# Kernel optimization log

Measured on AMD Instinct MI355X. Metric: run time of the kernel, lower is better.

Reference implementation:

```python
import jax, jax.numpy as jnp
import numpy as np

V, E, H, L = 10000, 256, 512, 2
B, T, S = 64, 64, 128
NEG = -1e6


def setup_inputs() -> dict:
    key = jax.random.key(0)
    ks = jax.random.split(key, 20)
    sc = 0.02
    inp = {
        "x": jax.random.randint(ks[0], (B, T), 0, V),
        "enc_outputs": jax.random.normal(ks[1], (B, S, H), jnp.float32),
        "h0": jax.random.normal(ks[2], (L, B, H), jnp.float32),
        "valid_lens": jax.random.randint(ks[3], (B,), 1, S + 1).astype(jnp.int32),
        # params
        "emb": jax.random.normal(ks[4], (V, E), jnp.float32) * sc,
        "Wq": jax.random.normal(ks[5], (H, H), jnp.float32) * sc,
        "Wk": jax.random.normal(ks[6], (H, H), jnp.float32) * sc,
        "wv": jax.random.normal(ks[7], (H,), jnp.float32) * sc,
        "W_ih0": jax.random.normal(ks[8], (3 * H, H + E), jnp.float32) * sc,
        "W_hh0": jax.random.normal(ks[9], (3 * H, H), jnp.float32) * sc,
        "b_ih0": jnp.zeros((3 * H,), jnp.float32),
        "b_hh0": jnp.zeros((3 * H,), jnp.float32),
        "W_ih1": jax.random.normal(ks[10], (3 * H, H), jnp.float32) * sc,
        "W_hh1": jax.random.normal(ks[11], (3 * H, H), jnp.float32) * sc,
        "b_ih1": jnp.zeros((3 * H,), jnp.float32),
        "b_hh1": jnp.zeros((3 * H,), jnp.float32),
        "Wd": jax.random.normal(ks[12], (V, H), jnp.float32) * sc,
        "bd": jnp.zeros((V,), jnp.float32),
    }
    return inp


def _gru_cell(x, h, W_ih, W_hh, b_ih, b_hh):
    # PyTorch GRU cell math
    gi = x @ W_ih.T + b_ih  # (B, 3H)
    gh = h @ W_hh.T + b_hh
    ir, iz, in_ = jnp.split(gi, 3, axis=-1)
    hr, hz, hn = jnp.split(gh, 3, axis=-1)
    r = jax.nn.sigmoid(ir + hr)
    z = jax.nn.sigmoid(iz + hz)
    n = jnp.tanh(in_ + r * hn)
    return (1.0 - z) * n + z * h


def reference(x, enc_outputs, h0, valid_lens, emb, Wq, Wk, wv,
              W_ih0, W_hh0, b_ih0, b_hh0, W_ih1, W_hh1, b_ih1, b_hh1, Wd, bd):
    X = emb[x]                     # (B, T, E)
    Xt = jnp.transpose(X, (1, 0, 2))  # (T, B, E) time-major
    k_proj = jnp.einsum('bsh,oh->bso', enc_outputs, Wk)  # precompute W_k(keys)
    mask = jnp.arange(S)[None, :] < valid_lens[:, None]  # (B, S)

    def step(h, x_t):
        q = h[-1]                                      # (B, H) last-layer hidden
        q_proj = q @ Wq.T                              # (B, H)
        feats = jnp.tanh(q_proj[:, None, :] + k_proj)  # (B, S, H)
        scores = jnp.einsum('bsh,h->bs', feats, wv)
        scores = jnp.where(mask, scores, NEG)
        attn = jax.nn.softmax(scores, axis=-1)
        context = jnp.einsum('bs,bsh->bh', attn, enc_outputs)
        inp = jnp.concatenate([context, x_t], axis=-1)  # (B, H+E)
        h0n = _gru_cell(inp, h[0], W_ih0, W_hh0, b_ih0, b_hh0)
        h1n = _gru_cell(h0n, h[1], W_ih1, W_hh1, b_ih1, b_hh1)
        hn = jnp.stack([h0n, h1n])
        return hn, h1n

    _, ys = jax.lax.scan(step, h0, Xt)       # ys: (T, B, H)
    logits = jnp.einsum('tbh,vh->tbv', ys, Wd) + bd
    return jnp.transpose(logits, (1, 0, 2))  # (B, T, V)
```

## Files before the change

kernel.cpp:

```cpp
#include <hip/hip_runtime.h>
#include <hip/hip_bf16.h>

#define Bd 64
#define Td 64
#define Sd 128
#define Hd 512
#define Ed 256
#define Vd 10000
#define NBLK 256

#define W0IH 0
#define W0HH 4608
#define W1IH 7680
#define W1HH 10752
#define WTOT 13824

typedef __attribute__((ext_vector_type(8))) short bf16x8;
typedef __attribute__((ext_vector_type(4))) float f32x4;

__device__ __forceinline__ float fast_tanh(float x) {
  float e = __expf(-2.0f * fabsf(x));
  float r = (1.0f - e) / (1.0f + e);
  return copysignf(r, x);
}
__device__ __forceinline__ float fast_sigmoid(float x) {
  return 1.0f / (1.0f + __expf(-x));
}
__device__ __forceinline__ float bf2f(unsigned short u) {
  return __uint_as_float(((unsigned int)u) << 16);
}
__device__ __forceinline__ void st_llc(float* p, float v) {
  __hip_atomic_store(p, v, __ATOMIC_RELAXED, __HIP_MEMORY_SCOPE_AGENT);
}
__device__ __forceinline__ int q4(int k, int b) {
  return (k >> 2) * 256 + b * 4 + (k & 3);
}

__device__ __forceinline__ void gbar(int* arrive, int* go, int ep, int blk, int tid) {
  __syncthreads();
  if (tid == 0)
    __hip_atomic_store(&arrive[blk], ep, __ATOMIC_RELAXED, __HIP_MEMORY_SCOPE_AGENT);
  if (blk == 0) {
    if (tid < 64) {
      for (;;) {
        int a0 = __hip_atomic_load(&arrive[tid], __ATOMIC_RELAXED,
                                   __HIP_MEMORY_SCOPE_AGENT);
        int a1 = __hip_atomic_load(&arrive[tid + 64], __ATOMIC_RELAXED,
                                   __HIP_MEMORY_SCOPE_AGENT);
        int a2 = __hip_atomic_load(&arrive[tid + 128], __ATOMIC_RELAXED,
                                   __HIP_MEMORY_SCOPE_AGENT);
        int a3 = __hip_atomic_load(&arrive[tid + 192], __ATOMIC_RELAXED,
                                   __HIP_MEMORY_SCOPE_AGENT);
        if (a0 >= ep && a1 >= ep && a2 >= ep && a3 >= ep) break;
        __builtin_amdgcn_s_sleep(2);
      }
    }
    __syncthreads();
    if (tid == 0)
      __hip_atomic_store(go, ep, __ATOMIC_RELAXED, __HIP_MEMORY_SCOPE_AGENT);
  }
  if (tid == 0) {
    while (__hip_atomic_load(go, __ATOMIC_RELAXED, __HIP_MEMORY_SCOPE_AGENT) < ep) {
      __builtin_amdgcn_s_sleep(1);
    }
    __builtin_amdgcn_fence(__ATOMIC_ACQUIRE, "agent");
  }
  __syncthreads();
}

__global__ void k_gemm_kp(const float* __restrict__ A, const float* __restrict__ W,
                          unsigned short* __restrict__ C, int M, int N, int K) {
  __shared__ __align__(16) float As[16][64];
  __shared__ __align__(16) float Ws[16][64];
  int m0 = blockIdx.x * 64, n0 = blockIdx.y * 64;
  int tid = threadIdx.x;
  int tx = tid & 15, ty = tid >> 4;
  float acc[4][4] = {};
  for (int k0 = 0; k0 < K; k0 += 16) {
#pragma unroll
    for (int i = 0; i < 4; i++) {
      int e = tid + i * 256;
      int r = e >> 4, c = e & 15;
      As[c][r] = A[(long)(m0 + r) * K + k0 + c];
      Ws[c][r] = W[(long)(n0 + r) * K + k0 + c];
    }
    __syncthreads();
#pragma unroll
    for (int k = 0; k < 16; k++) {
      float a_[4], w_[4];
#pragma unroll
      for (int i = 0; i < 4; i++) a_[i] = As[k][ty * 4 + i];
#pragma unroll
      for (int j = 0; j < 4; j++) w_[j] = Ws[k][tx * 4 + j];
#pragma unroll
      for (int i = 0; i < 4; i++)
#pragma unroll
        for (int j = 0; j < 4; j++) acc[i][j] += a_[i] * w_[j];
    }
    __syncthreads();
  }
#pragma unroll
  for (int i = 0; i < 4; i++)
#pragma unroll
    for (int j = 0; j < 4; j++) {
      __hip_bfloat16 h = __float2bfloat16(acc[i][j]);
      C[(long)(m0 + ty * 4 + i) * N + n0 + tx * 4 + j] = *(unsigned short*)&h;
    }
}

__global__ __launch_bounds__(256) void k_logits(
    const unsigned short* __restrict__ ysbf, const unsigned short* __restrict__ Wdbf,
    const float* __restrict__ bd, float* __restrict__ out, int N) {
  int m0 = blockIdx.x * 64, n0 = blockIdx.y * 64;
  int w = threadIdx.x >> 6, lane = threadIdx.x & 63;
  int row = lane & 15, kg = lane >> 4;
  int mw = m0 + w * 16;
  f32x4 acc[4] = {};
  const unsigned short* Arow = ysbf + (size_t)(mw + row) * 512 + kg * 8;
  for (int k0 = 0; k0 < 512; k0 += 32) {
    bf16x8 af = *(const bf16x8*)(Arow + k0);
#pragma unroll
    for (int nn = 0; nn < 4; nn++) {
      int ncol = n0 + nn * 16 + row;
      bf16x8 bfv = {};
      if (ncol < N) bfv = *(const bf16x8*)(Wdbf + (size_t)ncol * 512 + k0 + kg * 8);
      acc[nn] = __builtin_amdgcn_mfma_f32_16x16x32_bf16(af, bfv, acc[nn], 0, 0, 0);
    }
  }
#pragma unroll
  for (int nn = 0; nn < 4; nn++) {
    int ncol = n0 + nn * 16 + row;
    if (ncol < N) {
      float bv = bd[ncol];
#pragma unroll
      for (int r = 0; r < 4; r++) {
        int mm = mw + kg * 4 + r;
        int t_ = mm >> 6, b_ = mm & 63;
        out[((size_t)(b_ * Td + t_)) * N + ncol] = acc[nn][r] + bv;
      }
    }
  }
}

__global__ void k_tobf(const float* __restrict__ src, unsigned short* __restrict__ dst,
                       long n) {
  long i = (long)blockIdx.x * 1024 + threadIdx.x;
  if (i < n) {
    __hip_bfloat16 h = __float2bfloat16(src[i]);
    dst[i] = *(unsigned short*)&h;
  }
}

__global__ void k_embT(const int* __restrict__ x, const float* __restrict__ emb,
                       float* __restrict__ embTf) {
  __shared__ int rows[64];
  int t = blockIdx.x;
  if (threadIdx.x < 64) rows[threadIdx.x] = x[threadIdx.x * Td + t];
  __syncthreads();
  int e = threadIdx.x;
  for (int b = 0; b < 64; b++) {
    embTf[(size_t)t * 16384 + q4(e, b)] = emb[(long)rows[b] * Ed + e];
  }
}

template <bool C0>
__device__ __forceinline__ void cell_phase(
    int blk, int tid, int t, const float* __restrict__ aT,
    const float* __restrict__ embTf, const float* __restrict__ hT,
    const float* wIH, const float* wHH, const float* __restrict__ bih,
    const float* __restrict__ bhh, const float* __restrict__ dscale,
    float* __restrict__ houtT, unsigned short* __restrict__ ysbf, float* scratch) {
  int lane = tid & 63;
  int w = tid >> 6;
  const int RIH = C0 ? 768 : 512;
  float* ps = scratch;
  float* psE = scratch + 1536;
  if (w < 12) {
    int p = w >> 1, h = w & 1;
    bool ih = p < 3;
    int g = ih ? p : p - 3;
    const float* A = (ih ? aT : hT) + h * 64 * 256;
    const float* w0;
    const float* w1;
    if (ih) {
      w0 = wIH + (size_t)(2 * g) * RIH + h * 256;
      w1 = w0 + RIH;
    } else {
      w0 = wHH + (size_t)(2 * g) * 512 + h * 256;
      w1 = w0 + 512;
    }
    float a0 = 0.f, a1 = 0.f;
#pragma unroll 16
    for (int k = 0; k < 256; k += 4) {
      float4 x0 = *(const float4*)&w0[k];
      float4 x1 = *(const float4*)&w1[k];
      float4 av = *(const float4*)&A[(k >> 2) * 256 + lane * 4];
      a0 += av.x * x0.x + av.y * x0.y + av.z * x0.z + av.w * x0.w;
      a1 += av.x * x1.x + av.y * x1.y + av.z * x1.z + av.w * x1.w;
    }
    if (C0 && ih) {
      float inv = 1.0f / dscale[lane];
      a0 *= inv;
      a1 *= inv;
    }
    int R0 = (ih ? 0 : 6) + 2 * g;
    ps[(R0 * 2 + h) * 64 + lane] = a0;
    ps[((R0 + 1) * 2 + h) * 64 + lane] = a1;
  } else if (C0 && w < 15) {
    int r0 = (w - 12) * 2;
    const float* w0 = wIH + (size_t)r0 * 768 + 512;
    const float* w1 = wIH + (size_t)(r0 + 1) * 768 + 512;
    const float* ef = embTf + (size_t)t * 16384;
    float a0 = 0.f, a1 = 0.f;
#pragma unroll 16
    for (int e = 0; e < 256; e += 4) {
      float4 x0 = *(const float4*)&w0[e];
      float4 x1 = *(const float4*)&w1[e];
      float4 ev = *(const float4*)&ef[(e >> 2) * 256 + lane * 4];
      a0 += ev.x * x0.x + ev.y * x0.y + ev.z * x0.z + ev.w * x0.w;
      a1 += ev.x * x1.x + ev.y * x1.y + ev.z * x1.z + ev.w * x1.w;
    }
    psE[r0 * 64 + lane] = a0;
    psE[(r0 + 1) * 64 + lane] = a1;
  }
  __syncthreads();
  if (tid < 128) {
    int jl = tid >> 6, b = tid & 63;
#define RD(R) (ps[((R)*2 + 0) * 64 + b] + ps[((R)*2 + 1) * 64 + b])
    float ir = RD(0 + jl);
    float iz = RD(2 + jl);
    float in = RD(4 + jl);
    if (C0) {
      ir += psE[(0 + jl) * 64 + b];
      iz += psE[(2 + jl) * 64 + b];
      in += psE[(4 + jl) * 64 + b];
    }
    float hr = RD(6 + jl);
    float hz = RD(8 + jl);
    float hn_ = RD(10 + jl);
#undef RD
    int j = blk * 2 + jl;
    float r = fast_sigmoid(ir + hr + bih[j] + bhh[j]);
    float z = fast_sigmoid(iz + hz + bih[Hd + j] + bhh[Hd + j]);
    float n = fast_tanh(in + bih[2 * Hd + j] + r * (hn_ + bhh[2 * Hd + j]));
    float hp = hT[q4(j, b)];
    float out = (1.f - z) * n + z * hp;
    st_llc(&houtT[q4(j, b)], out);
    if (!C0) {
      __hip_bfloat16 hb = __float2bfloat16(out);
      ysbf[((size_t)t * 64 + b) * 512 + j] = *(unsigned short*)&hb;
    }
  }
}

__global__ __launch_bounds__(1024, 1) void k_decoder(
    const float* __restrict__ h0_in, const int* __restrict__ vlen,
    const float* __restrict__ Wq, const float* __restrict__ wvp,
    const float* __restrict__ Wih0, const float* __restrict__ Whh0,
    const float* __restrict__ bih0, const float* __restrict__ bhh0,
    const float* __restrict__ Wih1, const float* __restrict__ Whh1,
    const float* __restrict__ bih1, const float* __restrict__ bhh1,
    const unsigned short* __restrict__ kpbf, const unsigned short* __restrict__ encbf,
    const float* __restrict__ embTf, int* bar, float* qpN, float* ctxT,
    float* den, float* h0TA, float* h0TB, float* h1TA, float* h1TB,
    unsigned short* ysbf) {
  __shared__ __align__(16) float wLDS[WTOT];
  __shared__ __align__(16) float WqL[1024];
  __shared__ __align__(16) unsigned short kpL[32 * 512];
  __shared__ __align__(16) unsigned short encL[32 * 512];
  __shared__ __align__(16) float scratch[1920];
  int blk = blockIdx.x, tid = threadIdx.x;
  int lane = tid & 63;
  int w = tid >> 6;
  int battn = blk >> 2, q = blk & 3;
  int* arrive = bar;
  int* go = bar + NBLK;
  int ep = 0;

  {
    int j0 = blk * 2;
#pragma unroll
    for (int rr = 0; rr < 6; rr++) {
      int g = rr >> 1, jl = rr & 1;
      int row = g * Hd + j0 + jl;
      const float* s0 = Wih0 + (size_t)row * 768;
      for (int k = tid; k < 768; k += 1024) wLDS[W0IH + rr * 768 + k] = s0[k];
      const float* s1 = Whh0 + (size_t)row * Hd;
      for (int k = tid; k < Hd; k += 1024) wLDS[W0HH + rr * 512 + k] = s1[k];
      const float* s2 = Wih1 + (size_t)row * Hd;
      for (int k = tid; k < Hd; k += 1024) wLDS[W1IH + rr * 512 + k] = s2[k];
      const float* s3 = Whh1 + (size_t)row * Hd;
      for (int k = tid; k < Hd; k += 1024) wLDS[W1HH + rr * 512 + k] = s3[k];
    }
    WqL[tid] = Wq[(size_t)(blk * 2 + (tid >> 9)) * Hd + (tid & 511)];
    const uint4* ksrc = (const uint4*)(kpbf + ((size_t)battn * Sd + q * 32) * Hd);
    const uint4* esrc = (const uint4*)(encbf + ((size_t)battn * Sd + q * 32) * Hd);
    uint4* kdst = (uint4*)kpL;
    uint4* edst = (uint4*)encL;
    for (int i = tid; i < 2048; i += 1024) {
      kdst[i] = ksrc[i];
      edst[i] = esrc[i];
    }
  }
  float wvr[8];
#pragma unroll
  for (int i = 0; i < 8; i++) wvr[i] = wvp[lane * 8 + i];

  if (blk < Bd) {
    int b = blk;
    for (int k = tid; k < Hd; k += 1024) {
      st_llc(&h0TA[q4(k, b)], h0_in[(0 * Bd + b) * Hd + k]);
      st_llc(&h1TA[q4(k, b)], h0_in[(1 * Bd + b) * Hd + k]);
    }
  }
  if (tid < 128) st_llc(&ctxT[blk * 128 + tid], 0.f);
  if (blk < Bd && tid == 128) st_llc(&den[blk], 0.f);
  gbar(arrive, go, ++ep, blk, tid);

  for (int t = 0; t < Td; t++) {
    const float* h0prev = (t & 1) ? h0TB : h0TA;
    float* h0next = (t & 1) ? h0TA : h0TB;
    const float* h1prev = (t & 1) ? h1TB : h1TA;
    float* h1next = (t & 1) ? h1TA : h1TB;

    {
      int rl = w >> 3, ks = w & 7;
      const float* qrow = &WqL[rl * 512 + ks * 64];
      const float* hp4 = h1prev + (ks * 16) * 256 + lane * 4;
      float acc = 0.f;
#pragma unroll
      for (int kk = 0; kk < 64; kk += 4) {
        float4 hv = *(const float4*)&hp4[(kk >> 2) * 256];
        acc += hv.x * qrow[kk] + hv.y * qrow[kk + 1] + hv.z * qrow[kk + 2] +
               hv.w * qrow[kk + 3];
      }
      scratch[w * 64 + lane] = acc;
      __syncthreads();
      if (tid < 128) {
        int rl2 = tid >> 6, b = tid & 63;
        float s = 0.f;
#pragma unroll
        for (int qq = 0; qq < 8; qq++) s += scratch[(rl2 * 8 + qq) * 64 + b];
        st_llc(&qpN[(size_t)b * 512 + blk * 2 + rl2], s);
      }
    }
    gbar(arrive, go, ++ep, blk, tid);

    {
      int b = battn;
      float* sc = scratch;
      float qv[8];
      const float* qb = qpN + (size_t)b * 512 + lane * 8;
#pragma unroll
      for (int i = 0; i < 8; i++) qv[i] = qb[i];
      int vl = vlen[b];
#pragma unroll
      for (int si = 0; si < 2; si++) {
        int sl = w * 2 + si;
        uint4 kw = *(const uint4*)&kpL[sl * 512 + lane * 8];
        float f0 = __uint_as_float(kw.x << 16);
        float f1 = __uint_as_float(kw.x & 0xffff0000u);
        float f2 = __uint_as_float(kw.y << 16);
        float f3 = __uint_as_float(kw.y & 0xffff0000u);
        float f4 = __uint_as_float(kw.z << 16);
        float f5 = __uint_as_float(kw.z & 0xffff0000u);
        float f6 = __uint_as_float(kw.w << 16);
        float f7 = __uint_as_float(kw.w & 0xffff0000u);
        float acc = wvr[0] * fast_tanh(qv[0] + f0) + wvr[1] * fast_tanh(qv[1] + f1) +
                    wvr[2] * fast_tanh(qv[2] + f2) + wvr[3] * fast_tanh(qv[3] + f3) +
                    wvr[4] * fast_tanh(qv[4] + f4) + wvr[5] * fast_tanh(qv[5] + f5) +
                    wvr[6] * fast_tanh(qv[6] + f6) + wvr[7] * fast_tanh(qv[7] + f7);
#pragma unroll
        for (int off = 1; off < 64; off <<= 1) acc += __shfl_xor(acc, off);
        if (lane == 0) {
          int s = q * 32 + sl;
          sc[sl] = (s < vl) ? __expf(acc) : 0.f;
        }
      }
      __syncthreads();
      if (tid < 32) {
        float p2 = sc[tid];
#pragma unroll
        for (int off = 1; off < 32; off <<= 1) p2 += __shfl_xor(p2, off, 32);
        if (tid == 0) atomicAdd(&den[b], p2);
      }
      if (tid < 512) {
        float acc = 0.f;
#pragma unroll 8
        for (int s = 0; s < 32; s++) acc += sc[s] * bf2f(encL[s * 512 + tid]);
        atomicAdd(&ctxT[q4(tid, b)], acc);
      }
    }
    gbar(arrive, go, ++ep, blk, tid);

    cell_phase<true>(blk, tid, t, ctxT, embTf, h0prev, wLDS + W0IH, wLDS + W0HH,
                     bih0, bhh0, den, h0next, nullptr, scratch);
    gbar(arrive, go, ++ep, blk, tid);

    if (tid < 128) st_llc(&ctxT[blk * 128 + tid], 0.f);
    if (blk < Bd && tid == 128) st_llc(&den[blk], 0.f);
    cell_phase<false>(blk, tid, t, h0next, nullptr, h1prev, wLDS + W1IH,
                      wLDS + W1HH, bih1, bhh1, nullptr, h1next, ysbf, scratch);
    gbar(arrive, go, ++ep, blk, tid);
  }
}

extern "C" void kernel_launch(void* const* d_in, const int* in_sizes, int n_in,
                              void* d_out, int out_size, void* d_ws, size_t ws_size,
                              hipStream_t stream) {
  const int* x = (const int*)d_in[0];
  const float* enc = (const float*)d_in[1];
  const float* h0 = (const float*)d_in[2];
  const int* vlen = (const int*)d_in[3];
  const float* emb = (const float*)d_in[4];
  const float* Wq = (const float*)d_in[5];
  const float* Wk = (const float*)d_in[6];
  const float* wv = (const float*)d_in[7];
  const float* W_ih0 = (const float*)d_in[8];
  const float* W_hh0 = (const float*)d_in[9];
  const float* b_ih0 = (const float*)d_in[10];
  const float* b_hh0 = (const float*)d_in[11];
  const float* W_ih1 = (const float*)d_in[12];
  const float* W_hh1 = (const float*)d_in[13];
  const float* b_ih1 = (const float*)d_in[14];
  const float* b_hh1 = (const float*)d_in[15];
  const float* Wd = (const float*)d_in[16];
  const float* bd = (const float*)d_in[17];
  float* out = (float*)d_out;

  char* p = (char*)d_ws;
  int* bar = (int*)p;
  p += 2048;
  unsigned short* kpbf = (unsigned short*)p;
  p += (size_t)Bd * Sd * Hd * 2;
  unsigned short* encbf = (unsigned short*)p;
  p += (size_t)Bd * Sd * Hd * 2;
  unsigned short* Wdbf = (unsigned short*)p;
  p += (size_t)Vd * Hd * 2;
  unsigned short* ysbf = (unsigned short*)p;
  p += (size_t)Td * Bd * Hd * 2;
  float* embTf = (float*)p;
  p += (size_t)Td * Ed * Bd * 4;
  float* qpN = (float*)p;   p += (size_t)Bd * Hd * 4;
  float* ctxT = (float*)p;  p += (size_t)Hd * Bd * 4;
  float* den = (float*)p;   p += 256;
  float* h0TA = (float*)p;  p += (size_t)Hd * Bd * 4;
  float* h0TB = (float*)p;  p += (size_t)Hd * Bd * 4;
  float* h1TA = (float*)p;  p += (size_t)Hd * Bd * 4;
  float* h1TB = (float*)p;

  hipMemsetAsync(bar, 0, 2048, stream);

  k_gemm_kp<<<dim3(128, 8), 256, 0, stream>>>(enc, Wk, kpbf, Bd * Sd, Hd, Hd);
  long nenc = (long)Bd * Sd * Hd;
  k_tobf<<<(nenc + 1023) / 1024, 1024, 0, stream>>>(enc, encbf, nenc);
  long nwd = (long)Vd * Hd;
  k_tobf<<<(nwd + 1023) / 1024, 1024, 0, stream>>>(Wd, Wdbf, nwd);
  k_embT<<<Td, 256, 0, stream>>>(x, emb, embTf);
  k_decoder<<<NBLK, 1024, 0, stream>>>(h0, vlen, Wq, wv, W_ih0, W_hh0, b_ih0,
                                       b_hh0, W_ih1, W_hh1, b_ih1, b_hh1, kpbf,
                                       encbf, embTf, bar, qpN, ctxT, den, h0TA,
                                       h0TB, h1TA, h1TB, ysbf);
  k_logits<<<dim3(64, 157), 256, 0, stream>>>(ysbf, Wdbf, bd, out, Vd);
}
```

Baseline: 4.208 ms.

## Compute query projection redundantly per block to drop a grid barrier

Each block now computes the full 512-wide query projection for its own batch row from a bf16 transposed copy of Wq, which a new prep kernel produces. This removes the distributed qpN write and one grid-wide barrier per timestep. The GRU cell matvec is also restructured: 8 waves each handle 6 rows over a quarter of K, with the attention denominator division applied after the reduction. The cost is redundant Wq reads from global/L2 in every block (four blocks per batch row do the same work), plus bf16 rounding of Wq.

```diff
diff --git a/kernel.cpp b/kernel.cpp
--- a/kernel.cpp
+++ b/kernel.cpp
@@ -151,6 +151,20 @@
   }
 }
 
+__global__ void k_wqT(const float* __restrict__ Wq, unsigned short* __restrict__ WqT) {
+  __shared__ float tile[64][65];
+  int bi = blockIdx.x, bj = blockIdx.y;
+  int tx = threadIdx.x & 63, ty = threadIdx.x >> 6;
+  for (int i = 0; i < 64; i += 4)
+    tile[ty + i][tx] = Wq[(size_t)(bi * 64 + ty + i) * 512 + bj * 64 + tx];
+  __syncthreads();
+  for (int i = 0; i < 64; i += 4) {
+    int r = ty + i;
+    __hip_bfloat16 h = __float2bfloat16(tile[tx][r]);
+    WqT[(size_t)(bj * 64 + r) * 512 + bi * 64 + tx] = *(unsigned short*)&h;
+  }
+}
+
 __global__ void k_embT(const int* __restrict__ x, const float* __restrict__ emb,
                        float* __restrict__ embTf) {
   __shared__ int rows[64];
@@ -168,77 +182,71 @@
     int blk, int tid, int t, const float* __restrict__ aT,
     const float* __restrict__ embTf, const float* __restrict__ hT,
     const float* wIH, const float* wHH, const float* __restrict__ bih,
-    const float* __restrict__ bhh, const float* __restrict__ dscale,
+    const float* __restrict__ bhh, const float* __restrict__ den,
     float* __restrict__ houtT, unsigned short* __restrict__ ysbf, float* scratch) {
   int lane = tid & 63;
   int w = tid >> 6;
   const int RIH = C0 ? 768 : 512;
   float* ps = scratch;
-  float* psE = scratch + 1536;
-  if (w < 12) {
-    int p = w >> 1, h = w & 1;
-    bool ih = p < 3;
-    int g = ih ? p : p - 3;
-    const float* A = (ih ? aT : hT) + h * 64 * 256;
-    const float* w0;
-    const float* w1;
-    if (ih) {
-      w0 = wIH + (size_t)(2 * g) * RIH + h * 256;
-      w1 = w0 + RIH;
-    } else {
-      w0 = wHH + (size_t)(2 * g) * 512 + h * 256;
-      w1 = w0 + 512;
-    }
-    float a0 = 0.f, a1 = 0.f;
-#pragma unroll 16
-    for (int k = 0; k < 256; k += 4) {
-      float4 x0 = *(const float4*)&w0[k];
-      float4 x1 = *(const float4*)&w1[k];
-      float4 av = *(const float4*)&A[(k >> 2) * 256 + lane * 4];
-      a0 += av.x * x0.x + av.y * x0.y + av.z * x0.z + av.w * x0.w;
-      a1 += av.x * x1.x + av.y * x1.y + av.z * x1.z + av.w * x1.w;
-    }
-    if (C0 && ih) {
-      float inv = 1.0f / dscale[lane];
-      a0 *= inv;
-      a1 *= inv;
-    }
-    int R0 = (ih ? 0 : 6) + 2 * g;
-    ps[(R0 * 2 + h) * 64 + lane] = a0;
-    ps[((R0 + 1) * 2 + h) * 64 + lane] = a1;
-  } else if (C0 && w < 15) {
-    int r0 = (w - 12) * 2;
-    const float* w0 = wIH + (size_t)r0 * 768 + 512;
-    const float* w1 = wIH + (size_t)(r0 + 1) * 768 + 512;
-    const float* ef = embTf + (size_t)t * 16384;
-    float a0 = 0.f, a1 = 0.f;
-#pragma unroll 16
-    for (int e = 0; e < 256; e += 4) {
-      float4 x0 = *(const float4*)&w0[e];
-      float4 x1 = *(const float4*)&w1[e];
-      float4 ev = *(const float4*)&ef[(e >> 2) * 256 + lane * 4];
-      a0 += ev.x * x0.x + ev.y * x0.y + ev.z * x0.z + ev.w * x0.w;
-      a1 += ev.x * x1.x + ev.y * x1.y + ev.z * x1.z + ev.w * x1.w;
-    }
-    psE[r0 * 64 + lane] = a0;
-    psE[(r0 + 1) * 64 + lane] = a1;
+  float* psE = scratch + 3072;
+  if (w < 8) {
+    int strm = w >> 2, qk = w & 3;
+    const float* A = (strm == 0 ? aT : hT) + qk * 32 * 256;
+    float a[6] = {0.f, 0.f, 0.f, 0.f, 0.f, 0.f};
+#pragma unroll 8
+    for (int k4 = 0; k4 < 32; k4++) {
+      float4 av = *(const float4*)&A[k4 * 256 + lane * 4];
+#pragma unroll
+      for (int r = 0; r < 6; r++) {
+        const float* wr = (strm == 0 ? wIH + (size_t)r * RIH : wHH + (size_t)r * 512) +
+                          qk * 128 + k4 * 4;
+        float4 w4 = *(const float4*)wr;
+        a[r] += av.x * w4.x + av.y * w4.y + av.z * w4.z + av.w * w4.w;
+      }
+    }
+    int base = strm * 6;
+#pragma unroll
+    for (int r = 0; r < 6; r++) ps[((base + r) * 4 + qk) * 64 + lane] = a[r];
+  } else if (C0 && w < 12) {
+    int qe = w - 8;
+    const float* ef = embTf + (size_t)t * 16384 + qe * 16 * 256;
+    float a[6] = {0.f, 0.f, 0.f, 0.f, 0.f, 0.f};
+#pragma unroll 8
+    for (int k4 = 0; k4 < 16; k4++) {
+      float4 ev = *(const float4*)&ef[k4 * 256 + lane * 4];
+#pragma unroll
+      for (int r = 0; r < 6; r++) {
+        const float* wr = wIH + (size_t)r * 768 + 512 + qe * 64 + k4 * 4;
+        float4 w4 = *(const float4*)wr;
+        a[r] += ev.x * w4.x + ev.y * w4.y + ev.z * w4.z + ev.w * w4.w;
+      }
+    }
+#pragma unroll
+    for (int r = 0; r < 6; r++) psE[(r * 4 + qe) * 64 + lane] = a[r];
   }
   __syncthreads();
   if (tid < 128) {
     int jl = tid >> 6, b = tid & 63;
-#define RD(R) (ps[((R)*2 + 0) * 64 + b] + ps[((R)*2 + 1) * 64 + b])
+    float invd = C0 ? (1.0f / den[b]) : 1.0f;
+#define RD(R)                                                              \
+  (ps[((R)*4 + 0) * 64 + b] + ps[((R)*4 + 1) * 64 + b] +                   \
+   ps[((R)*4 + 2) * 64 + b] + ps[((R)*4 + 3) * 64 + b])
+#define RE(R)                                                              \
+  (psE[((R)*4 + 0) * 64 + b] + psE[((R)*4 + 1) * 64 + b] +                 \
+   psE[((R)*4 + 2) * 64 + b] + psE[((R)*4 + 3) * 64 + b])
     float ir = RD(0 + jl);
     float iz = RD(2 + jl);
     float in = RD(4 + jl);
     if (C0) {
-      ir += psE[(0 + jl) * 64 + b];
-      iz += psE[(2 + jl) * 64 + b];
-      in += psE[(4 + jl) * 64 + b];
+      ir = ir * invd + RE(0 + jl);
+      iz = iz * invd + RE(2 + jl);
+      in = in * invd + RE(4 + jl);
     }
     float hr = RD(6 + jl);
     float hz = RD(8 + jl);
     float hn_ = RD(10 + jl);
 #undef RD
+#undef RE
     int j = blk * 2 + jl;
     float r = fast_sigmoid(ir + hr + bih[j] + bhh[j]);
     float z = fast_sigmoid(iz + hz + bih[Hd + j] + bhh[Hd + j]);
@@ -255,20 +263,19 @@
 
 __global__ __launch_bounds__(1024, 1) void k_decoder(
     const float* __restrict__ h0_in, const int* __restrict__ vlen,
-    const float* __restrict__ Wq, const float* __restrict__ wvp,
+    const unsigned short* __restrict__ WqTbf, const float* __restrict__ wvp,
     const float* __restrict__ Wih0, const float* __restrict__ Whh0,
     const float* __restrict__ bih0, const float* __restrict__ bhh0,
     const float* __restrict__ Wih1, const float* __restrict__ Whh1,
     const float* __restrict__ bih1, const float* __restrict__ bhh1,
     const unsigned short* __restrict__ kpbf, const unsigned short* __restrict__ encbf,
-    const float* __restrict__ embTf, int* bar, float* qpN, float* ctxT,
-    float* den, float* h0TA, float* h0TB, float* h1TA, float* h1TB,
-    unsigned short* ysbf) {
+    const float* __restrict__ embTf, int* bar, float* ctxT, float* den,
+    float* h0TA, float* h0TB, float* h1TA, float* h1TB, unsigned short* ysbf) {
   __shared__ __align__(16) float wLDS[WTOT];
-  __shared__ __align__(16) float WqL[1024];
   __shared__ __align__(16) unsigned short kpL[32 * 512];
   __shared__ __align__(16) unsigned short encL[32 * 512];
-  __shared__ __align__(16) float scratch[1920];
+  __shared__ __align__(16) float scratch[4608];
+  __shared__ __align__(16) float h1s[512];
   int blk = blockIdx.x, tid = threadIdx.x;
   int lane = tid & 63;
   int w = tid >> 6;
@@ -292,7 +299,6 @@
       const float* s3 = Whh1 + (size_t)row * Hd;
       for (int k = tid; k < Hd; k += 1024) wLDS[W1HH + rr * 512 + k] = s3[k];
     }
-    WqL[tid] = Wq[(size_t)(blk * 2 + (tid >> 9)) * Hd + (tid & 511)];
     const uint4* ksrc = (const uint4*)(kpbf + ((size_t)battn * Sd + q * 32) * Hd);
     const uint4* esrc = (const uint4*)(encbf + ((size_t)battn * Sd + q * 32) * Hd);
     uint4* kdst = (uint4*)kpL;
@@ -324,35 +330,42 @@
     float* h1next = (t & 1) ? h1TA : h1TB;
 
     {
-      int rl = w >> 3, ks = w & 7;
-      const float* qrow = &WqL[rl * 512 + ks * 64];
-      const float* hp4 = h1prev + (ks * 16) * 256 + lane * 4;
-      float acc = 0.f;
-#pragma unroll
-      for (int kk = 0; kk < 64; kk += 4) {
-        float4 hv = *(const float4*)&hp4[(kk >> 2) * 256];
-        acc += hv.x * qrow[kk] + hv.y * qrow[kk + 1] + hv.z * qrow[kk + 2] +
-               hv.w * qrow[kk + 3];
-      }
-      scratch[w * 64 + lane] = acc;
+      int b = battn;
+      if (tid < 512) h1s[tid] = h1prev[q4(tid, b)];
       __syncthreads();
-      if (tid < 128) {
-        int rl2 = tid >> 6, b = tid & 63;
+      float* qpP = scratch;
+      float* qpF = scratch + 4096;
+      if (w < 8) {
+        float p[8] = {0.f, 0.f, 0.f, 0.f, 0.f, 0.f, 0.f, 0.f};
+        const unsigned short* Wt = WqTbf + (size_t)(w * 64) * 512 + lane * 8;
+#pragma unroll 8
+        for (int kk = 0; kk < 64; kk++) {
+          float hv = h1s[w * 64 + kk];
+          uint4 u = *(const uint4*)(Wt + (size_t)kk * 512);
+          p[0] += hv * __uint_as_float(u.x << 16);
+          p[1] += hv * __uint_as_float(u.x & 0xffff0000u);
+          p[2] += hv * __uint_as_float(u.y << 16);
+          p[3] += hv * __uint_as_float(u.y & 0xffff0000u);
+          p[4] += hv * __uint_as_float(u.z << 16);
+          p[5] += hv * __uint_as_float(u.z & 0xffff0000u);
+          p[6] += hv * __uint_as_float(u.w << 16);
+          p[7] += hv * __uint_as_float(u.w & 0xffff0000u);
+        }
+#pragma unroll
+        for (int i = 0; i < 8; i++) qpP[w * 512 + lane * 8 + i] = p[i];
+      }
+      __syncthreads();
+      if (tid < 512) {
         float s = 0.f;
 #pragma unroll
-        for (int qq = 0; qq < 8; qq++) s += scratch[(rl2 * 8 + qq) * 64 + b];
-        st_llc(&qpN[(size_t)b * 512 + blk * 2 + rl2], s);
-      }
-    }
-    gbar(arrive, go, ++ep, blk, tid);
-
-    {
-      int b = battn;
-      float* sc = scratch;
+        for (int ww = 0; ww < 8; ww++) s += qpP[ww * 512 + tid];
+        qpF[tid] = s;
+      }
+      __syncthreads();
       float qv[8];
-      const float* qb = qpN + (size_t)b * 512 + lane * 8;
-#pragma unroll
-      for (int i = 0; i < 8; i++) qv[i] = qb[i];
+#pragma unroll
+      for (int i = 0; i < 8; i++) qv[i] = qpF[lane * 8 + i];
+      float* sc = scratch + 4608 - 640;
       int vl = vlen[b];
 #pragma unroll
       for (int si = 0; si < 2; si++) {
@@ -437,11 +450,12 @@
   p += (size_t)Bd * Sd * Hd * 2;
   unsigned short* Wdbf = (unsigned short*)p;
   p += (size_t)Vd * Hd * 2;
+  unsigned short* WqTbf = (unsigned short*)p;
+  p += (size_t)Hd * Hd * 2;
   unsigned short* ysbf = (unsigned short*)p;
   p += (size_t)Td * Bd * Hd * 2;
   float* embTf = (float*)p;
   p += (size_t)Td * Ed * Bd * 4;
-  float* qpN = (float*)p;   p += (size_t)Bd * Hd * 4;
   float* ctxT = (float*)p;  p += (size_t)Hd * Bd * 4;
   float* den = (float*)p;   p += 256;
   float* h0TA = (float*)p;  p += (size_t)Hd * Bd * 4;
@@ -456,10 +470,11 @@
   k_tobf<<<(nenc + 1023) / 1024, 1024, 0, stream>>>(enc, encbf, nenc);
   long nwd = (long)Vd * Hd;
   k_tobf<<<(nwd + 1023) / 1024, 1024, 0, stream>>>(Wd, Wdbf, nwd);
+  k_wqT<<<dim3(8, 8), 256, 0, stream>>>(Wq, WqTbf);
   k_embT<<<Td, 256, 0, stream>>>(x, emb, embTf);
-  k_decoder<<<NBLK, 1024, 0, stream>>>(h0, vlen, Wq, wv, W_ih0, W_hh0, b_ih0,
+  k_decoder<<<NBLK, 1024, 0, stream>>>(h0, vlen, WqTbf, wv, W_ih0, W_hh0, b_ih0,
                                        b_hh0, W_ih1, W_hh1, b_ih1, b_hh1, kpbf,
-                                       encbf, embTf, bar, qpN, ctxT, den, h0TA,
-                                       h0TB, h1TA, h1TB, ysbf);
+                                       encbf, embTf, bar, ctxT, den, h0TA, h0TB,
+                                       h1TA, h1TB, ysbf);
   k_logits<<<dim3(64, 157), 256, 0, stream>>>(ysbf, Wdbf, bd, out, Vd);
 }
```

Measured after the change: 4.500 ms. 1.07x slower.
